# Performance work log

Hardware: AMD Instinct MI355X
Metric: run time of the kernel (lower is better)

Reference implementation:

```python
import jax, jax.numpy as jnp
import numpy as np

N = 12288
IN_F = 256
OUT_F = 128
SLOPE = 0.2
MASK_VAL = -9e16


def setup_inputs() -> dict:
    key = jax.random.key(0)
    k1, k2, k3, k4 = jax.random.split(key, 4)
    h = jax.random.normal(k1, (N, IN_F), dtype=jnp.float32)
    adj_matrix = jax.random.randint(k2, (N, N), 0, 2, dtype=jnp.int32)
    W = jax.random.normal(k3, (IN_F, OUT_F), dtype=jnp.float32) * (1.0 / np.sqrt(IN_F))
    a = jax.random.normal(k4, (2 * OUT_F, 1), dtype=jnp.float32) * (1.0 / np.sqrt(2 * OUT_F))
    return {"h": h, "adj_matrix": adj_matrix, "W": W, "a": a}


def reference(h, adj_matrix, W, a):
    # eval mode: F.dropout is identity
    h_t = h @ W                              # [N, OUT_F]
    src = h_t @ a[:OUT_F]                    # [N, 1]
    tgt = h_t @ a[OUT_F:]                    # [N, 1]
    e = src + tgt.T                          # [N, N] additive scores
    e = jnp.where(e >= 0, e, SLOPE * e)      # leaky relu
    e = jnp.where(adj_matrix > 0, e, MASK_VAL)
    attention = jax.nn.softmax(e, axis=-1)   # [N, N]
    h_prime = attention @ h_t                # [N, OUT_F]
    return (h_prime, attention)
```

## Files before the change

### kernel.cpp

```cpp
#include <hip/hip_runtime.h>
#include <hip/hip_bf16.h>
#include <stdint.h>

#define NN 12288
#define INF_ 256
#define OUTF 128
#define SLOPE 0.2f

typedef __bf16 bf16x8 __attribute__((ext_vector_type(8)));
typedef float f32x16 __attribute__((ext_vector_type(16)));
typedef float f32x4 __attribute__((ext_vector_type(4)));
typedef uint32_t u32x4 __attribute__((ext_vector_type(4)));

union BFU { u32x4 u; bf16x8 b; };

__device__ __forceinline__ float bflo(uint32_t u){ return __uint_as_float(u << 16); }
__device__ __forceinline__ float bfhi(uint32_t u){ return __uint_as_float(u & 0xffff0000u); }
__device__ __forceinline__ uint32_t f2bf(float f){
    union { __bf16 b; uint16_t s; } u; u.b = (__bf16)f; return (uint32_t)u.s;
}
__device__ __forceinline__ void unpack8(u32x4 u, float* f){
    f[0]=bflo(u.x); f[1]=bfhi(u.x); f[2]=bflo(u.y); f[3]=bfhi(u.y);
    f[4]=bflo(u.z); f[5]=bfhi(u.z); f[6]=bflo(u.w); f[7]=bfhi(u.w);
}

__global__ __launch_bounds__(256) void k0_detect(const uint32_t* __restrict__ hw,
                                                 uint32_t* __restrict__ flag)
{
    __shared__ int cnt[4];
    int t = threadIdx.x;
    uint32_t w = hw[t];
    uint32_t e = (w >> 7) & 0xffu;
    int s = (e >= 110u && e <= 140u) ? 1 : 0;
    #pragma unroll
    for (int mm=1;mm<64;mm<<=1) s += __shfl_xor(s,mm,64);
    if ((t&63)==0) cnt[t>>6]=s;
    __syncthreads();
    if (t==0) flag[0] = ((cnt[0]+cnt[1]+cnt[2]+cnt[3]) < 128) ? 1u : 0u;
}

__global__ __launch_bounds__(256) void k1_ht(
    const void* __restrict__ h, const void* __restrict__ Wp,
    const void* __restrict__ a, const uint32_t* __restrict__ flagp,
    uint16_t* __restrict__ packed, float* __restrict__ src, float* __restrict__ tgt)
{
    __shared__ __align__(16) uint16_t tile[16*128];
    int t = threadIdx.x;
    int rloc = t >> 4;
    int row = blockIdx.x*16 + rloc;
    int f0 = (t & 15) * 8;
    bool f32in = flagp[0] != 0u;

    float acc[8];
    #pragma unroll
    for (int c=0;c<8;c++) acc[c]=0.f;
    float a1f[8], a2f[8];

    if (f32in){
        const float* hrow = (const float*)h + (size_t)row*INF_;
        const float* Wf   = (const float*)Wp;
        for (int k=0;k<INF_;k+=8){
            float hv[8];
            *(f32x4*)&hv[0] = *(const f32x4*)(hrow + k);
            *(f32x4*)&hv[4] = *(const f32x4*)(hrow + k + 4);
            #pragma unroll
            for (int i=0;i<8;i++){
                const float* w0 = Wf + (size_t)(k+i)*OUTF + f0;
                float wf[8];
                *(f32x4*)&wf[0] = *(const f32x4*)w0;
                *(f32x4*)&wf[4] = *(const f32x4*)(w0+4);
                #pragma unroll
                for (int c=0;c<8;c++) acc[c] = fmaf(hv[i], wf[c], acc[c]);
            }
        }
        const float* af = (const float*)a;
        *(f32x4*)&a1f[0] = *(const f32x4*)(af + f0);
        *(f32x4*)&a1f[4] = *(const f32x4*)(af + f0 + 4);
        *(f32x4*)&a2f[0] = *(const f32x4*)(af + OUTF + f0);
        *(f32x4*)&a2f[4] = *(const f32x4*)(af + OUTF + f0 + 4);
    } else {
        const uint16_t* hrow = (const uint16_t*)h + (size_t)row*INF_;
        const uint16_t* W16  = (const uint16_t*)Wp;
        for (int k=0;k<INF_;k+=8){
            u32x4 hu = *(const u32x4*)(hrow + k);
            float hv[8]; unpack8(hu,hv);
            #pragma unroll
            for (int i=0;i<8;i++){
                u32x4 wu = *(const u32x4*)(W16 + (size_t)(k+i)*OUTF + f0);
                float wf[8]; unpack8(wu,wf);
                #pragma unroll
                for (int c=0;c<8;c++) acc[c] = fmaf(hv[i], wf[c], acc[c]);
            }
        }
        const uint16_t* a16 = (const uint16_t*)a;
        u32x4 a1u = *(const u32x4*)(a16 + f0);
        u32x4 a2u = *(const u32x4*)(a16 + OUTF + f0);
        unpack8(a1u,a1f); unpack8(a2u,a2f);
    }

    float p1=0.f, p2=0.f;
    #pragma unroll
    for (int c=0;c<8;c++){ p1 = fmaf(acc[c],a1f[c],p1); p2 = fmaf(acc[c],a2f[c],p2); }
    #pragma unroll
    for (int mm=1;mm<16;mm<<=1){ p1 += __shfl_xor(p1,mm,64); p2 += __shfl_xor(p2,mm,64); }
    if ((t&15)==0){ src[row]=p1; tgt[row]=p2; }

    uint32_t q0 = f2bf(acc[0]) | (f2bf(acc[1])<<16);
    uint32_t q1 = f2bf(acc[2]) | (f2bf(acc[3])<<16);
    uint32_t q2 = f2bf(acc[4]) | (f2bf(acc[5])<<16);
    uint32_t q3 = f2bf(acc[6]) | (f2bf(acc[7])<<16);
    u32x4 pk = {q0,q1,q2,q3};
    *(u32x4*)&tile[rloc*128 + f0] = pk;
    __syncthreads();
    int n = t >> 1, kb = (t & 1) * 8;
    uint32_t g0 = (uint32_t)tile[(kb+0)*128+n] | ((uint32_t)tile[(kb+1)*128+n]<<16);
    uint32_t g1 = (uint32_t)tile[(kb+2)*128+n] | ((uint32_t)tile[(kb+3)*128+n]<<16);
    uint32_t g2 = (uint32_t)tile[(kb+4)*128+n] | ((uint32_t)tile[(kb+5)*128+n]<<16);
    uint32_t g3 = (uint32_t)tile[(kb+6)*128+n] | ((uint32_t)tile[(kb+7)*128+n]<<16);
    u32x4 ov = {g0,g1,g2,g3};
    *(u32x4*)(packed + (size_t)blockIdx.x*2048 + t*8) = ov;
}

__global__ __launch_bounds__(256) void k1b_max(const float* __restrict__ tgt,
                                               float* __restrict__ maxtgt)
{
    __shared__ float red[4];
    int t = threadIdx.x;
    float m = -3.4e38f;
    for (int j=t; j<NN; j+=256) m = fmaxf(m, tgt[j]);
    #pragma unroll
    for (int mm=1;mm<64;mm<<=1) m = fmaxf(m, __shfl_xor(m,mm,64));
    if ((t&63)==0) red[t>>6]=m;
    __syncthreads();
    if (t==0) maxtgt[0] = fmaxf(fmaxf(red[0],red[1]), fmaxf(red[2],red[3]));
}

__global__ __launch_bounds__(256) void k2_mask(
    const int* __restrict__ adj, const float* __restrict__ src,
    const float* __restrict__ maxtgt, const float* __restrict__ tgt,
    uint32_t* __restrict__ bm, float* __restrict__ Mrow, float* __restrict__ Srow)
{
    __shared__ float ls[4];
    int row = blockIdx.x, t = threadIdx.x;
    float sr = src[row];
    float e0 = sr + maxtgt[0];
    float M  = fmaxf(e0, SLOPE*e0);
    const u32x4* arow = (const u32x4*)(adj + (size_t)row*NN);
    uint32_t* bmrow = bm + (size_t)row*384;
    float sum = 0.f;
    #pragma unroll
    for (int jb=0;jb<12;jb++){
        int j0 = jb*1024 + t*4;
        u32x4 a4 = __builtin_nontemporal_load(arow + jb*256 + t);
        float4 t4 = *(const float4*)(tgt + j0);
        uint32_t nib = (a4.x!=0u) | ((a4.y!=0u)<<1) | ((a4.z!=0u)<<2) | ((a4.w!=0u)<<3);
        float ev, lv, pv;
        ev = sr + t4.x; lv = fmaxf(ev, SLOPE*ev); pv = __expf(lv - M); sum += (nib&1u)     ? pv : 0.f;
        ev = sr + t4.y; lv = fmaxf(ev, SLOPE*ev); pv = __expf(lv - M); sum += ((nib>>1)&1u)? pv : 0.f;
        ev = sr + t4.z; lv = fmaxf(ev, SLOPE*ev); pv = __expf(lv - M); sum += ((nib>>2)&1u)? pv : 0.f;
        ev = sr + t4.w; lv = fmaxf(ev, SLOPE*ev); pv = __expf(lv - M); sum += ((nib>>3)&1u)? pv : 0.f;
        uint32_t wv = nib << ((t&7)*4);
        wv |= __shfl_xor(wv,1,64); wv |= __shfl_xor(wv,2,64); wv |= __shfl_xor(wv,4,64);
        if ((t&7)==0) __builtin_nontemporal_store(wv, bmrow + jb*32 + (t>>3));
    }
    #pragma unroll
    for (int mm=1;mm<64;mm<<=1) sum += __shfl_xor(sum,mm,64);
    if ((t&63)==0) ls[t>>6]=sum;
    __syncthreads();
    if (t==0){ Srow[row] = ls[0]+ls[1]+ls[2]+ls[3]; Mrow[row] = M; }
}

__global__ __launch_bounds__(256) void k3_pv(
    const uint32_t* __restrict__ bm, const float* __restrict__ tgt,
    const float* __restrict__ src, const float* __restrict__ Mrow,
    const float* __restrict__ Srow, const uint16_t* __restrict__ packed,
    const uint32_t* __restrict__ flagp, void* __restrict__ out)
{
    __shared__ __align__(16) uint16_t P[32*136];
    int t = threadIdx.x;
    int lane = t & 63, wv = t >> 6;
    int r0 = blockIdx.x * 32;
    int rr0 = t >> 4;
    int jg  = t & 15; int jl0 = jg*8;
    int n0 = wv*32;
    int m = lane & 31, kq = lane >> 5;
    bool f32out = flagp[0] != 0u;

    uint16_t* hprime16 = (uint16_t*)out;
    uint16_t* attn16   = hprime16 + (size_t)NN*OUTF;
    float*    hprimef  = (float*)out;
    float*    attnf    = hprimef + (size_t)NN*OUTF;

    float s0 = src[r0+rr0],      s1 = src[r0+rr0+16];
    float M0 = Mrow[r0+rr0],     M1 = Mrow[r0+rr0+16];
    float S0 = Srow[r0+rr0],     S1 = Srow[r0+rr0+16];
    float inv0 = S0>0.f ? 1.f/S0 : 0.f;  float fb0 = S0>0.f ? 0.f : 1.f/NN;
    float inv1 = S1>0.f ? 1.f/S1 : 0.f;  float fb1 = S1>0.f ? 0.f : 1.f/NN;

    f32x16 acc;
    #pragma unroll
    for (int i=0;i<16;i++) acc[i]=0.f;

    for (int c=0;c<NN/128;c++){
        int jbase = c*128;
        float tg[8];
        *(f32x4*)&tg[0] = *(const f32x4*)(tgt + jbase + jl0);
        *(f32x4*)&tg[4] = *(const f32x4*)(tgt + jbase + jl0 + 4);
        #pragma unroll
        for (int hh=0;hh<2;hh++){
            int rr = rr0 + hh*16;
            uint32_t word = bm[(size_t)(r0+rr)*384 + (c<<2) + (jg>>2)];
            uint32_t byt  = (word >> ((jg&3)*8)) & 0xffu;
            float sv = hh? s1:s0, Mv = hh? M1:M0, iv = hh? inv1:inv0, fv = hh? fb1:fb0;
            uint32_t pk[4];
            float pf[8];
            #pragma unroll
            for (int i=0;i<4;i++){
                float ea = sv + tg[2*i],   eb = sv + tg[2*i+1];
                float la = fmaxf(ea, SLOPE*ea), lb = fmaxf(eb, SLOPE*eb);
                float pa = ((byt>>(2*i))&1u)   ? __expf(la-Mv)*iv : fv;
                float pb = ((byt>>(2*i+1))&1u) ? __expf(lb-Mv)*iv : fv;
                pk[i] = f2bf(pa) | (f2bf(pb)<<16);
                pf[2*i] = pa; pf[2*i+1] = pb;
            }
            u32x4 pv4 = {pk[0],pk[1],pk[2],pk[3]};
            if (f32out){
                f32x4 fa = {pf[0],pf[1],pf[2],pf[3]};
                f32x4 fb = {pf[4],pf[5],pf[6],pf[7]};
                float* dst = attnf + (size_t)(r0+rr)*NN + jbase + jl0;
                __builtin_nontemporal_store(fa, (f32x4*)dst);
                __builtin_nontemporal_store(fb, (f32x4*)(dst+4));
            } else {
                __builtin_nontemporal_store(pv4,
                    (u32x4*)(attn16 + (size_t)(r0+rr)*NN + jbase + jl0));
            }
            *(u32x4*)&P[rr*136 + jl0] = pv4;
        }
        __syncthreads();
        #pragma unroll
        for (int kt=0;kt<8;kt++){
            BFU A; A.u = *(const u32x4*)&P[m*136 + (kt<<4) + (kq<<3)];
            BFU B; B.u = *(const u32x4*)(packed +
                        (((size_t)(c*8+kt))<<11) + ((size_t)(n0+m)<<4) + (kq<<3));
            acc = __builtin_amdgcn_mfma_f32_32x32x16_bf16(A.b, B.b, acc, 0, 0, 0);
        }
        __syncthreads();
    }
    #pragma unroll
    for (int r=0;r<16;r++){
        int orow = (r&3) + 8*(r>>2) + 4*kq;
        if (f32out) hprimef [(size_t)(r0+orow)*OUTF + n0 + m] = acc[r];
        else        hprime16[(size_t)(r0+orow)*OUTF + n0 + m] = (uint16_t)f2bf(acc[r]);
    }
}

extern "C" void kernel_launch(void* const* d_in, const int* in_sizes, int n_in,
                              void* d_out, int out_size, void* d_ws, size_t ws_size,
                              hipStream_t stream)
{
    const void* h  = d_in[0];
    const int*  adj= (const int*)d_in[1];
    const void* W  = d_in[2];
    const void* a  = d_in[3];

    char* ws = (char*)d_ws;
    uint16_t* packed = (uint16_t*)ws;
    float* src    = (float*)(ws + 3145728);
    float* tgt    = (float*)(ws + 3194880);
    float* Mrow   = (float*)(ws + 3244032);
    float* Srow   = (float*)(ws + 3293184);
    float* maxtgt = (float*)(ws + 3342336);
    uint32_t* flag= (uint32_t*)(ws + 3342400);
    uint32_t* bm  = (uint32_t*)(ws + 3342464);

    k0_detect<<<dim3(1),    dim3(256), 0, stream>>>((const uint32_t*)h, flag);
    k1_ht    <<<dim3(NN/16),dim3(256), 0, stream>>>(h, W, a, flag, packed, src, tgt);
    k1b_max  <<<dim3(1),    dim3(256), 0, stream>>>(tgt, maxtgt);
    k2_mask  <<<dim3(NN),   dim3(256), 0, stream>>>(adj, src, maxtgt, tgt, bm, Mrow, Srow);
    k3_pv    <<<dim3(NN/32),dim3(256), 0, stream>>>(bm, tgt, src, Mrow, Srow, packed, flag, d_out);
}
```

Measured before the change: 1.153 ms.

## Split k3 attention-PV over key dimension with atomic fp32 accumulation

The PV kernel's grid gains a second dimension that splits the key columns into 8 chunks, so there are 8x more blocks (384 to 3072) to fill the GPU's compute units. Partial h' results are atomically added into a zeroed fp32 workspace buffer. A new finalize kernel then converts that buffer to the output dtype. This adds a zeroing kernel, a finalize kernel, atomic traffic and nondeterministic summation order in exchange for better occupancy.

```diff
diff --git a/kernel.cpp b/kernel.cpp
--- a/kernel.cpp
+++ b/kernel.cpp
@@ -6,6 +6,8 @@
 #define INF_ 256
 #define OUTF 128
 #define SLOPE 0.2f
+#define JSPLIT 8
+#define CPB (NN/128/JSPLIT)
 
 typedef __bf16 bf16x8 __attribute__((ext_vector_type(8)));
 typedef float f32x16 __attribute__((ext_vector_type(16)));
@@ -135,6 +137,13 @@
     if (t==0) maxtgt[0] = fmaxf(fmaxf(red[0],red[1]), fmaxf(red[2],red[3]));
 }
 
+__global__ __launch_bounds__(256) void k1c_zero(float* __restrict__ hp)
+{
+    int i = blockIdx.x*256 + threadIdx.x;
+    f32x4 z = {0.f,0.f,0.f,0.f};
+    *(f32x4*)(hp + (size_t)i*4) = z;
+}
+
 __global__ __launch_bounds__(256) void k2_mask(
     const int* __restrict__ adj, const float* __restrict__ src,
     const float* __restrict__ maxtgt, const float* __restrict__ tgt,
@@ -174,7 +183,8 @@
     const uint32_t* __restrict__ bm, const float* __restrict__ tgt,
     const float* __restrict__ src, const float* __restrict__ Mrow,
     const float* __restrict__ Srow, const uint16_t* __restrict__ packed,
-    const uint32_t* __restrict__ flagp, void* __restrict__ out)
+    const uint32_t* __restrict__ flagp, float* __restrict__ hp,
+    void* __restrict__ out)
 {
     __shared__ __align__(16) uint16_t P[32*136];
     int t = threadIdx.x;
@@ -201,7 +211,8 @@
     #pragma unroll
     for (int i=0;i<16;i++) acc[i]=0.f;
 
-    for (int c=0;c<NN/128;c++){
+    int cs = blockIdx.y * CPB;
+    for (int c=cs; c<cs+CPB; c++){
         int jbase = c*128;
         float tg[8];
         *(f32x4*)&tg[0] = *(const f32x4*)(tgt + jbase + jl0);
@@ -249,8 +260,29 @@
     #pragma unroll
     for (int r=0;r<16;r++){
         int orow = (r&3) + 8*(r>>2) + 4*kq;
-        if (f32out) hprimef [(size_t)(r0+orow)*OUTF + n0 + m] = acc[r];
-        else        hprime16[(size_t)(r0+orow)*OUTF + n0 + m] = (uint16_t)f2bf(acc[r]);
+        atomicAdd(&hp[(size_t)(r0+orow)*OUTF + n0 + m], acc[r]);
+    }
+}
+
+__global__ __launch_bounds__(256) void k4_fin(const float* __restrict__ hp,
+    const uint32_t* __restrict__ flagp, void* __restrict__ out)
+{
+    int t = blockIdx.x*256 + threadIdx.x;
+    size_t base = (size_t)t*8;
+    bool f32out = flagp[0] != 0u;
+    f32x4 v0 = *(const f32x4*)(hp + base);
+    f32x4 v1 = *(const f32x4*)(hp + base + 4);
+    if (f32out){
+        float* o = (float*)out;
+        *(f32x4*)(o + base)     = v0;
+        *(f32x4*)(o + base + 4) = v1;
+    } else {
+        uint32_t q0 = f2bf(v0.x) | (f2bf(v0.y)<<16);
+        uint32_t q1 = f2bf(v0.z) | (f2bf(v0.w)<<16);
+        uint32_t q2 = f2bf(v1.x) | (f2bf(v1.y)<<16);
+        uint32_t q3 = f2bf(v1.z) | (f2bf(v1.w)<<16);
+        u32x4 pk = {q0,q1,q2,q3};
+        *(u32x4*)((uint16_t*)out + base) = pk;
     }
 }
 
@@ -272,10 +304,14 @@
     float* maxtgt = (float*)(ws + 3342336);
     uint32_t* flag= (uint32_t*)(ws + 3342400);
     uint32_t* bm  = (uint32_t*)(ws + 3342464);
+    float* hp     = (float*)(ws + 22216832);
 
     k0_detect<<<dim3(1),    dim3(256), 0, stream>>>((const uint32_t*)h, flag);
     k1_ht    <<<dim3(NN/16),dim3(256), 0, stream>>>(h, W, a, flag, packed, src, tgt);
     k1b_max  <<<dim3(1),    dim3(256), 0, stream>>>(tgt, maxtgt);
+    k1c_zero <<<dim3(NN*OUTF/1024), dim3(256), 0, stream>>>(hp);
     k2_mask  <<<dim3(NN),   dim3(256), 0, stream>>>(adj, src, maxtgt, tgt, bm, Mrow, Srow);
-    k3_pv    <<<dim3(NN/32),dim3(256), 0, stream>>>(bm, tgt, src, Mrow, Srow, packed, flag, d_out);
-}
+    k3_pv    <<<dim3(NN/32, JSPLIT), dim3(256), 0, stream>>>(bm, tgt, src, Mrow, Srow,
+                                                             packed, flag, hp, d_out);
+    k4_fin   <<<dim3(NN*OUTF/2048), dim3(256), 0, stream>>>(hp, flag, d_out);
+}
```

After: 1.134 ms. No clear change (-1.6%).
